# Performance work log

Measured on AMD Instinct MI355X. Metric: run time of the kernel, lower is better.

## Reference

```python
import jax, jax.numpy as jnp
import numpy as np

B, N = 16, 4096

def _fps(xyz, npoint):
    # iterative farthest point sampling on one cloud [n,3] -> [npoint] int32
    n = xyz.shape[0]
    def body(carry, _):
        dist, far = carry
        d = jnp.sum((xyz - xyz[far]) ** 2, axis=-1)
        dist = jnp.minimum(dist, d)
        return (dist, jnp.argmax(dist).astype(jnp.int32)), far
    _, idx = jax.lax.scan(body, (jnp.full((n,), 1e10, jnp.float32), jnp.int32(0)), None, length=npoint)
    return idx

def _ball_query(radius, nsample, xyz, new_xyz):
    # xyz [n,3], new_xyz [S,3] -> [S,nsample] neighbor indices (first-in-index order, as in PointNet++)
    n = xyz.shape[0]
    sqr = jnp.sum((new_xyz[:, None, :] - xyz[None, :, :]) ** 2, axis=-1)  # [S,n]
    idx = jnp.where(sqr > radius * radius, n, jnp.arange(n, dtype=jnp.int32)[None, :])
    idx = jnp.sort(idx, axis=-1)[:, :nsample]
    return jnp.where(idx == n, idx[:, :1], idx)

def _gather(p, i):
    return jax.vmap(lambda pp, ii: pp[ii])(p, i)

def _mlp(x, layers):
    # shared MLP = 1x1 conv over grouped points; BN(eval) folded into (W,b)
    for W, b in layers:
        x = jax.nn.relu(jnp.einsum('bsnc,co->bsno', x, W) + b)
    return x

def _sa(xyz, feats, npoint, radius, nsample, layers):
    fps_idx = jax.vmap(lambda p: _fps(p, npoint))(xyz)            # [B,S]
    new_xyz = _gather(xyz, fps_idx)                                # [B,S,3]
    idx = jax.vmap(lambda p, q: _ball_query(radius, nsample, p, q))(xyz, new_xyz)  # [B,S,ns]
    x = _gather(xyz, idx) - new_xyz[:, :, None, :]                 # centered grouped xyz
    if feats is not None:
        x = jnp.concatenate([x, _gather(feats, idx)], axis=-1)
    x = _mlp(x, layers)
    return new_xyz, jnp.max(x, axis=2)

def _forward(points, w10, b10, w11, b11, w12, b12, w20, b20, w21, b21, w22, b22, w30, b30, w31, b31, w32, b32, lw1, lb1, lw2, lb2, fw1, fb1, fw2, fb2, pos_mean, pos_std, rot_mean, rot_std):
    l1x, l1f = _sa(points, None, 512, 0.2, 32, [(w10, b10), (w11, b11), (w12, b12)])
    l2x, l2f = _sa(l1x, l1f, 128, 0.4, 64, [(w20, b20), (w21, b21), (w22, b22)])
    # sa3: group_all
    x = jnp.concatenate([l2x, l2f], axis=-1)[:, None]              # [B,1,128,259]
    x = _mlp(x, [(w30, b30), (w31, b31), (w32, b32)])
    g = jnp.max(x, axis=2).reshape(points.shape[0], 1024)
    label = jax.nn.sigmoid(jax.nn.relu(g @ lw1 + lb1) @ lw2 + lb2)  # dropout = identity (eval)
    res = jax.nn.relu(g @ fw1 + fb1) @ fw2 + fb2
    pl = res[:, 0:3] * pos_std + pos_mean
    rl = res[:, 3:9] * rot_std + rot_mean
    pr = res[:, 9:12] * pos_std + pos_mean
    rr = res[:, 12:18] * rot_std + rot_mean
    return jnp.concatenate([label, pl, rl, pr, rr], axis=-1)       # [B,20]

def setup_inputs():
    ks = iter(jax.random.split(jax.random.key(0), 64))
    def w(shape, s=0.05):
        return jax.random.normal(next(ks), shape, jnp.float32) * s
    inp = {'points': jax.random.normal(next(ks), (B, N, 3), jnp.float32) * 0.5}
    dims = {'w10': (3, 64), 'w11': (64, 64), 'w12': (64, 128), 'w20': (131, 128), 'w21': (128, 128), 'w22': (128, 256), 'w30': (259, 256), 'w31': (256, 512), 'w32': (512, 1024), 'lw1': (1024, 256), 'lw2': (256, 2), 'fw1': (1024, 512), 'fw2': (512, 18)}
    for name, s in dims.items():
        inp[name] = w(s)
        inp[name.replace('w', 'b', 1)] = jnp.zeros((s[1],), jnp.float32)
    inp['pos_mean'] = w((3,), 0.1)
    inp['pos_std'] = jnp.abs(w((3,))) + 1.0
    inp['rot_mean'] = w((6,), 0.1)
    inp['rot_std'] = jnp.abs(w((6,))) + 1.0
    return inp

def reference(points, w10, b10, w11, b11, w12, b12, w20, b20, w21, b21, w22, b22, w30, b30, w31, b31, w32, b32, lw1, lb1, lw2, lb2, fw1, fb1, fw2, fb2, pos_mean, pos_std, rot_mean, rot_std):
    return _forward(points, w10, b10, w11, b11, w12, b12, w20, b20, w21, b21, w22, b22, w30, b30, w31, b31, w32, b32, lw1, lb1, lw2, lb2, fw1, fb1, fw2, fb2, pos_mean, pos_std, rot_mean, rot_std)
```

## Files before the change

### kernel.cpp

```cpp
#include <hip/hip_runtime.h>
#include <math.h>

#define BB 16
#define NN 4096

typedef float v2f __attribute__((ext_vector_type(2)));
typedef short bfrag8 __attribute__((ext_vector_type(8)));
typedef float fx4 __attribute__((ext_vector_type(4)));

__device__ __forceinline__ v2f pkfma(v2f a, v2f b, v2f c) {
    return __builtin_elementwise_fma(a, b, c);
}

__device__ __forceinline__ fx4 mfma16(bfrag8 a, bfrag8 b, fx4 c) {
    return __builtin_amdgcn_mfma_f32_16x16x32_bf16(a, b, c, 0, 0, 0);
}

__device__ __forceinline__ unsigned short bf16rne(float v) {
    unsigned u = __float_as_uint(v);
    return (unsigned short)((u + 0x7FFFu + ((u >> 16) & 1u)) >> 16);
}
__device__ __forceinline__ void bf16split(float v, unsigned short& h, unsigned short& l) {
    h = bf16rne(v);
    float fh = __uint_as_float((unsigned)h << 16);
    l = bf16rne(v - fh);
}

__device__ __forceinline__ float sq3(float dx, float dy, float dz) {
    return __fadd_rn(__fadd_rn(__fmul_rn(dx, dx), __fmul_rn(dy, dy)), __fmul_rn(dz, dz));
}

template<int CTRL, int RMASK>
__device__ __forceinline__ unsigned long long dpp_max_step(unsigned long long P) {
    int lo = __builtin_amdgcn_update_dpp(0, (int)(unsigned)P,        CTRL, RMASK, 0xf, true);
    int hi = __builtin_amdgcn_update_dpp(0, (int)(unsigned)(P >> 32), CTRL, RMASK, 0xf, true);
    unsigned long long o = ((unsigned long long)(unsigned)hi << 32) | (unsigned)lo;
    return (o > P) ? o : P;
}

__device__ __forceinline__ unsigned long long dpp_wave_max_u64(unsigned long long P) {
    P = dpp_max_step<0x111, 0xf>(P);
    P = dpp_max_step<0x112, 0xf>(P);
    P = dpp_max_step<0x114, 0xf>(P);
    P = dpp_max_step<0x118, 0xf>(P);
    P = dpp_max_step<0x142, 0xa>(P);
    P = dpp_max_step<0x143, 0xc>(P);
    return P;
}

__device__ __forceinline__ unsigned long long u64max(unsigned long long a, unsigned long long b) {
    return (a > b) ? a : b;
}

template<int NPTS, int NPOINT, int TPB>
__global__ __launch_bounds__(TPB) void fps_kernel(const float* __restrict__ xyz,
                                                  float* __restrict__ newxyz,
                                                  float* __restrict__ out_t,
                                                  int ts) {
    constexpr int PPT = NPTS / TPB;
    constexpr int NW  = TPB / 64;
    static_assert(NPOINT <= TPB, "far-history latch needs NPOINT <= TPB");
    __shared__ float sx[NPTS], sy[NPTS], sz[NPTS];
    __shared__ __align__(16) unsigned long long slot[2][NW];
    const int b = blockIdx.x;
    const int tid = threadIdx.x;
    const float* base = xyz + (size_t)b * NPTS * 3;
    for (int i = tid; i < NPTS; i += TPB) {
        sx[i] = base[i * 3 + 0];
        sy[i] = base[i * 3 + 1];
        sz[i] = base[i * 3 + 2];
    }
    __syncthreads();
    float px[PPT], py[PPT], pz[PPT], dist[PPT];
#pragma unroll
    for (int k = 0; k < PPT; k++) {
        int p = tid + k * TPB;
        px[k] = sx[p]; py[k] = sy[p]; pz[k] = sz[p];
        dist[k] = 1e10f;
    }
    int far = 0;
    int myfar = 0;
    const int lane = tid & 63, wid = tid >> 6;
    for (int it = 0; it < NPOINT; it++) {
        if (tid == it) myfar = far;
        float fx = sx[far], fy = sy[far], fz = sz[far];
        float bv = -1.0f; int bi = 0;
#pragma unroll
        for (int k = 0; k < PPT; k++) {
            float d = sq3(px[k] - fx, py[k] - fy, pz[k] - fz);
            float nd = fminf(dist[k], d);
            dist[k] = nd;
            if (nd > bv) { bv = nd; bi = tid + k * TPB; }
        }
        unsigned long long P = ((unsigned long long)__float_as_uint(bv) << 32)
                             | (unsigned long long)(~(unsigned)bi & 0xFFFFFFFFull);
        P = dpp_wave_max_u64(P);
        int bufi = it & 1;
        if (lane == 63) slot[bufi][wid] = P;
        __syncthreads();
        unsigned long long v[NW];
#pragma unroll
        for (int w = 0; w < NW; w++) v[w] = slot[bufi][w];
#pragma unroll
        for (int st = NW / 2; st >= 1; st >>= 1)
#pragma unroll
            for (int w = 0; w < st; w++) v[w] = u64max(v[w], v[w + st]);
        far = (int)(~(unsigned)(v[0] & 0xFFFFFFFFull));
    }
    if (tid < NPOINT) {
        float fx = sx[myfar], fy = sy[myfar], fz = sz[myfar];
        newxyz[((size_t)b * NPOINT + tid) * 3 + 0] = fx;
        newxyz[((size_t)b * NPOINT + tid) * 3 + 1] = fy;
        newxyz[((size_t)b * NPOINT + tid) * 3 + 2] = fz;
        if (out_t) {
            out_t[0 * ts + b * NPOINT + tid] = fx;
            out_t[1 * ts + b * NPOINT + tid] = fy;
            out_t[2 * ts + b * NPOINT + tid] = fz;
        }
    }
}

template<int NS>
__device__ __forceinline__ void bq_body(const float* __restrict__ pts, int n,
                                        const float* __restrict__ centers, int S,
                                        float r2, int* __restrict__ outidx,
                                        int wave, int lane) {
    int b = wave / S, s = wave % S;
    const float* c = centers + ((size_t)b * S + s) * 3;
    float cx = c[0], cy = c[1], cz = c[2];
    const float* pb = pts + (size_t)b * n * 3;
    int* out = outidx + ((size_t)b * S + s) * NS;
    int total = 0, first = -1;
    int rounds = n >> 6;
    for (int r = 0; r < rounds; r++) {
        int p = (r << 6) + lane;
        float dx = pb[p * 3 + 0] - cx, dy = pb[p * 3 + 1] - cy, dz = pb[p * 3 + 2] - cz;
        float d = sq3(dx, dy, dz);
        bool pred = (d <= r2);
        unsigned long long mask = __ballot(pred);
        if (first < 0 && mask) first = (r << 6) + (__ffsll(mask) - 1);
        if (pred) {
            int rank = total + __popcll(mask & ((1ull << lane) - 1ull));
            if (rank < NS) out[rank] = p;
        }
        total += __popcll(mask);
        if (total >= NS) break;
    }
    for (int j = total + lane; j < NS; j += 64) out[j] = first;
}

__global__ __launch_bounds__(512) void bq1_fps2_kernel(const float* __restrict__ points,
                                                       const float* __restrict__ l1x,
                                                       float* __restrict__ l2x,
                                                       float* __restrict__ x3t,
                                                       int* __restrict__ idx1,
                                                       float r2a,
                                                       const float* __restrict__ w21,
                                                       const float* __restrict__ w22,
                                                       float* __restrict__ w21f,
                                                       float* __restrict__ w22f) {
    __shared__ float sx[512], sy[512], sz[512];
    const int tid = threadIdx.x;
    const int lane = tid & 63, wid = tid >> 6;
    if (blockIdx.x < 16) {
        if (wid != 0) return;
        const int b = blockIdx.x;
        const float* base = l1x + (size_t)b * 512 * 3;
        for (int i = lane; i < 512; i += 64) {
            sx[i] = base[i * 3 + 0];
            sy[i] = base[i * 3 + 1];
            sz[i] = base[i * 3 + 2];
        }
        float px[8], py[8], pz[8], dist[8];
#pragma unroll
        for (int k = 0; k < 8; k++) {
            int p = lane + k * 64;
            px[k] = sx[p]; py[k] = sy[p]; pz[k] = sz[p];
            dist[k] = 1e10f;
        }
        int far = 0, myfar0 = 0, myfar1 = 0;
        for (int it = 0; it < 128; it++) {
            if (lane == it) myfar0 = far;
            if (lane == it - 64) myfar1 = far;
            float fx = sx[far], fy = sy[far], fz = sz[far];
            float bv = -1.0f; int bi = 0;
#pragma unroll
            for (int k = 0; k < 8; k++) {
                float d = sq3(px[k] - fx, py[k] - fy, pz[k] - fz);
                float nd = fminf(dist[k], d);
                dist[k] = nd;
                if (nd > bv) { bv = nd; bi = lane + k * 64; }
            }
            unsigned long long P = ((unsigned long long)__float_as_uint(bv) << 32)
                                 | (unsigned long long)(~(unsigned)bi & 0xFFFFFFFFull);
            P = dpp_wave_max_u64(P);
            unsigned lo = (unsigned)__builtin_amdgcn_readlane((int)(unsigned)P, 63);
            far = (int)(~lo);
        }
        {
            int s0 = lane, s1 = lane + 64;
            float a = sx[myfar0], c1 = sy[myfar0], c2 = sz[myfar0];
            l2x[((size_t)b * 128 + s0) * 3 + 0] = a;
            l2x[((size_t)b * 128 + s0) * 3 + 1] = c1;
            l2x[((size_t)b * 128 + s0) * 3 + 2] = c2;
            x3t[0 * 2048 + b * 128 + s0] = a;
            x3t[1 * 2048 + b * 128 + s0] = c1;
            x3t[2 * 2048 + b * 128 + s0] = c2;
            float d = sx[myfar1], e = sy[myfar1], f = sz[myfar1];
            l2x[((size_t)b * 128 + s1) * 3 + 0] = d;
            l2x[((size_t)b * 128 + s1) * 3 + 1] = e;
            l2x[((size_t)b * 128 + s1) * 3 + 2] = f;
            x3t[0 * 2048 + b * 128 + s1] = d;
            x3t[1 * 2048 + b * 128 + s1] = e;
            x3t[2 * 2048 + b * 128 + s1] = f;
        }
    } else if (blockIdx.x < 1040) {
        int wave = (blockIdx.x - 16) * 8 + wid;
        bq_body<32>(points, 4096, l1x, 512, r2a, idx1, wave, lane);
    } else {
        int gt = (blockIdx.x - 1040) * 512 + tid;
        const float* W; float* OF; int NT, N; int t;
        if (gt < 4096) { W = w21; OF = w21f; NT = 8;  N = 128; t = gt; }
        else           { W = w22; OF = w22f; NT = 16; N = 256; t = gt - 4096; }
        int L = t & 63;
        int rest = t >> 6;
        int nt = rest & (NT - 1);
        int hk = (NT == 8) ? (rest >> 3) : (rest >> 4);
        int kt = hk & 3, hl = hk >> 2;
        int k0 = kt * 32 + (L >> 4) * 8;
        int n  = nt * 16 + (L & 15);
        unsigned o[4];
#pragma unroll
        for (int e = 0; e < 4; e++) {
            float va = W[(size_t)(k0 + 2 * e + 0) * N + n];
            float vb = W[(size_t)(k0 + 2 * e + 1) * N + n];
            unsigned short ha, la, hb, lb;
            bf16split(va, ha, la);
            bf16split(vb, hb, lb);
            o[e] = hl ? ((unsigned)la | ((unsigned)lb << 16))
                      : ((unsigned)ha | ((unsigned)hb << 16));
        }
        ((uint4*)OF)[t] = make_uint4(o[0], o[1], o[2], o[3]);
    }
}

__global__ __launch_bounds__(64, 2) void sa1_bq2_kernel(const float* __restrict__ xyz, const float* __restrict__ l1x,
                                                 const int* __restrict__ idx1,
                                                 const float* __restrict__ l2x, int* __restrict__ idx2, float r2b,
                                                 const float* __restrict__ W1, const float* __restrict__ B1,
                                                 const float* __restrict__ W2, const float* __restrict__ B2,
                                                 const float* __restrict__ W3, const float* __restrict__ B3,
                                                 float* __restrict__ l1f) {
    __shared__ float ht[64 * 64];
    int lane = threadIdx.x;
    if (blockIdx.x < 2048) {
        bq_body<64>(l1x, 512, l2x, 128, r2b, idx2, blockIdx.x, lane);
        return;
    }
    int blk = blockIdx.x - 2048;
    int b = blk >> 8;
    int s = ((blk & 255) << 1) | (lane >> 5);
    int nn = lane & 31;
    int center = b * 512 + s;
    int ii = idx1[center * 32 + nn];
    float px = xyz[((size_t)b * NN + ii) * 3 + 0] - l1x[(size_t)center * 3 + 0];
    float py = xyz[((size_t)b * NN + ii) * 3 + 1] - l1x[(size_t)center * 3 + 1];
    float pz = xyz[((size_t)b * NN + ii) * 3 + 2] - l1x[(size_t)center * 3 + 2];
#pragma unroll
    for (int c = 0; c < 64; c++)
        ht[c * 64 + lane] = fmaxf(B1[c] + px * W1[c] + py * W1[64 + c] + pz * W1[128 + c], 0.0f);
    __syncthreads();
    v2f h2[32];
    const v2f* B2v = (const v2f*)B2;
#pragma unroll
    for (int c = 0; c < 32; c++) h2[c] = B2v[c];
    for (int k = 0; k < 64; k++) {
        float xk = ht[k * 64 + lane];
        v2f xk2 = {xk, xk};
        const v2f* wr = (const v2f*)(W2 + k * 64);
#pragma unroll
        for (int c = 0; c < 32; c++) h2[c] = pkfma(xk2, wr[c], h2[c]);
    }
    __syncthreads();
#pragma unroll
    for (int c = 0; c < 32; c++) {
        ht[(2 * c + 0) * 64 + lane] = fmaxf(h2[c].x, 0.0f);
        ht[(2 * c + 1) * 64 + lane] = fmaxf(h2[c].y, 0.0f);
    }
    __syncthreads();
#pragma unroll
    for (int half = 0; half < 2; half++) {
        v2f o[32];
        const v2f* B3v = (const v2f*)(B3 + half * 64);
#pragma unroll
        for (int j = 0; j < 32; j++) o[j] = B3v[j];
        for (int k = 0; k < 64; k++) {
            float xk = ht[k * 64 + lane];
            v2f xk2 = {xk, xk};
            const v2f* wr = (const v2f*)(W3 + k * 128 + half * 64);
#pragma unroll
            for (int j = 0; j < 32; j++) o[j] = pkfma(xk2, wr[j], o[j]);
        }
#pragma unroll
        for (int j = 0; j < 32; j++) {
            float va = fmaxf(o[j].x, 0.0f);
            float vb = fmaxf(o[j].y, 0.0f);
#pragma unroll
            for (int m = 16; m >= 1; m >>= 1) {
                va = fmaxf(va, __shfl_xor(va, m));
                vb = fmaxf(vb, __shfl_xor(vb, m));
            }
            o[j].x = va; o[j].y = vb;
        }
        if (nn == 0) {
#pragma unroll
            for (int j = 0; j < 32; j++) {
                l1f[(size_t)center * 128 + half * 64 + 2 * j + 0] = o[j].x;
                l1f[(size_t)center * 128 + half * 64 + 2 * j + 1] = o[j].y;
            }
        }
    }
}

__global__ __launch_bounds__(256, 4) void sa2_kernel(const float* __restrict__ l1x, const float* __restrict__ l2x,
                                                  const float* __restrict__ l1f, const int* __restrict__ idx2,
                                                  const float* __restrict__ W1, const float* __restrict__ B1,
                                                  const float* __restrict__ w21f, const float* __restrict__ B2,
                                                  const float* __restrict__ w22f, const float* __restrict__ B3,
                                                  float* __restrict__ x3t) {
    __shared__ short hsh[64 * 136];
    __shared__ short hsl[64 * 136];
    int tid = threadIdx.x;
    int w = __builtin_amdgcn_readfirstlane(tid >> 6);
    int lane = tid & 63;
    int b = blockIdx.x >> 7, s = blockIdx.x & 127;
    int center = b * 128 + s;
    int ii = idx2[center * 64 + lane];
    float cx = l2x[(size_t)center * 3 + 0], cy = l2x[(size_t)center * 3 + 1], cz = l2x[(size_t)center * 3 + 2];
    const float* pr = l1x + ((size_t)b * 512 + ii) * 3;
    float px = pr[0] - cx, py = pr[1] - cy, pz = pr[2] - cz;
    const float4* frow = (const float4*)(l1f + ((size_t)b * 512 + ii) * 128);
    v2f h[16];
    {
        const v2f* B1v = (const v2f*)(B1 + w * 32);
        const v2f* w1a = (const v2f*)(W1 + 0 * 128 + w * 32);
        const v2f* w1b = (const v2f*)(W1 + 1 * 128 + w * 32);
        const v2f* w1c = (const v2f*)(W1 + 2 * 128 + w * 32);
        v2f px2 = {px, px}, py2 = {py, py}, pz2 = {pz, pz};
#pragma unroll
        for (int j = 0; j < 16; j++)
            h[j] = pkfma(pz2, w1c[j], pkfma(py2, w1b[j], pkfma(px2, w1a[j], B1v[j])));
    }
#pragma unroll 2
    for (int k4 = 0; k4 < 32; k4++) {
        float4 f = frow[k4];
        const v2f* wr = (const v2f*)(W1 + (3 + k4 * 4) * 128 + w * 32);
        v2f fx2 = {f.x, f.x}, fy2 = {f.y, f.y}, fz2 = {f.z, f.z}, fw2 = {f.w, f.w};
#pragma unroll
        for (int j = 0; j < 16; j++) {
            h[j] = pkfma(fx2, wr[j], h[j]);
            h[j] = pkfma(fy2, wr[64 + j], h[j]);
            h[j] = pkfma(fz2, wr[128 + j], h[j]);
            h[j] = pkfma(fw2, wr[192 + j], h[j]);
        }
    }
#pragma unroll
    for (int j = 0; j < 16; j++) {
        float v0 = fmaxf(h[j].x, 0.0f);
        float v1 = fmaxf(h[j].y, 0.0f);
        unsigned short h0, l0, h1, l1;
        bf16split(v0, h0, l0);
        bf16split(v1, h1, l1);
        int cb = lane * 136 + w * 32 + 2 * j;
        *(unsigned*)(&hsh[cb]) = (unsigned)h0 | ((unsigned)h1 << 16);
        *(unsigned*)(&hsl[cb]) = (unsigned)l0 | ((unsigned)l1 << 16);
    }
    __syncthreads();
    {
        fx4 acc[4][2];
#pragma unroll
        for (int mt = 0; mt < 4; mt++)
#pragma unroll
            for (int nt = 0; nt < 2; nt++) {
                float bn = B2[(2 * w + nt) * 16 + (lane & 15)];
                acc[mt][nt] = (fx4){bn, bn, bn, bn};
            }
#pragma unroll
        for (int kt = 0; kt < 4; kt++) {
            bfrag8 ah[4], al[4];
#pragma unroll
            for (int mt = 0; mt < 4; mt++) {
                int idx = (mt * 16 + (lane & 15)) * 136 + kt * 32 + (lane >> 4) * 8;
                ah[mt] = *(const bfrag8*)(&hsh[idx]);
                al[mt] = *(const bfrag8*)(&hsl[idx]);
            }
#pragma unroll
            for (int nt = 0; nt < 2; nt++) {
                int ng = 2 * w + nt;
                bfrag8 bh = ((const bfrag8*)w21f)[(size_t)((0 + kt) * 8 + ng) * 64 + lane];
                bfrag8 bl = ((const bfrag8*)w21f)[(size_t)((4 + kt) * 8 + ng) * 64 + lane];
#pragma unroll
                for (int mt = 0; mt < 4; mt++) {
                    acc[mt][nt] = mfma16(ah[mt], bh, acc[mt][nt]);
                    acc[mt][nt] = mfma16(ah[mt], bl, acc[mt][nt]);
                    acc[mt][nt] = mfma16(al[mt], bh, acc[mt][nt]);
                }
            }
        }
        __syncthreads();
#pragma unroll
        for (int mt = 0; mt < 4; mt++)
#pragma unroll
            for (int nt = 0; nt < 2; nt++)
#pragma unroll
                for (int r = 0; r < 4; r++) {
                    float v = fmaxf(acc[mt][nt][r], 0.0f);
                    int m = mt * 16 + (lane >> 4) * 4 + r;
                    int n = (2 * w + nt) * 16 + (lane & 15);
                    unsigned short hb, lb;
                    bf16split(v, hb, lb);
                    hsh[m * 136 + n] = (short)hb;
                    hsl[m * 136 + n] = (short)lb;
                }
        __syncthreads();
    }
#pragma unroll 1
    for (int pass = 0; pass < 2; pass++) {
        int nb = w * 4 + pass * 2;
        fx4 acc[4][2];
#pragma unroll
        for (int mt = 0; mt < 4; mt++)
#pragma unroll
            for (int nt = 0; nt < 2; nt++) {
                float bn = B3[(nb + nt) * 16 + (lane & 15)];
                acc[mt][nt] = (fx4){bn, bn, bn, bn};
            }
#pragma unroll
        for (int kt = 0; kt < 4; kt++) {
            bfrag8 ah[4], al[4];
#pragma unroll
            for (int mt = 0; mt < 4; mt++) {
                int idx = (mt * 16 + (lane & 15)) * 136 + kt * 32 + (lane >> 4) * 8;
                ah[mt] = *(const bfrag8*)(&hsh[idx]);
                al[mt] = *(const bfrag8*)(&hsl[idx]);
            }
#pragma unroll
            for (int nt = 0; nt < 2; nt++) {
                bfrag8 bh = ((const bfrag8*)w22f)[(size_t)((0 + kt) * 16 + (nb + nt)) * 64 + lane];
                bfrag8 bl = ((const bfrag8*)w22f)[(size_t)((4 + kt) * 16 + (nb + nt)) * 64 + lane];
#pragma unroll
                for (int mt = 0; mt < 4; mt++) {
                    acc[mt][nt] = mfma16(ah[mt], bh, acc[mt][nt]);
                    acc[mt][nt] = mfma16(ah[mt], bl, acc[mt][nt]);
                    acc[mt][nt] = mfma16(al[mt], bh, acc[mt][nt]);
                }
            }
        }
#pragma unroll
        for (int nt = 0; nt < 2; nt++) {
            float mv = 0.0f;
#pragma unroll
            for (int mt = 0; mt < 4; mt++)
#pragma unroll
                for (int r = 0; r < 4; r++)
                    mv = fmaxf(mv, acc[mt][nt][r]);
            mv = fmaxf(mv, __shfl_xor(mv, 16));
            mv = fmaxf(mv, __shfl_xor(mv, 32));
            if (lane < 16)
                x3t[(size_t)(3 + (nb + nt) * 16 + lane) * 2048 + center] = mv;
        }
    }
}

template<int K, int COUT, int CPT, bool MAXOUT>
__device__ __forceinline__ void gemm_t_body(const float* __restrict__ in_t,
                                            const float* __restrict__ W,
                                            const float* __restrict__ bias,
                                            float* __restrict__ outp,
                                            int bid, int lane) {
    int rw = bid & 31, cg = bid >> 5;
    int row = rw * 64 + lane;
    int cbase = cg * CPT;
    v2f acc[CPT / 2];
    const v2f* bv = (const v2f*)(bias + cbase);
#pragma unroll
    for (int j = 0; j < CPT / 2; j++) acc[j] = bv[j];
    for (int k = 0; k < K; k++) {
        float xk = in_t[(size_t)k * 2048 + row];
        v2f xk2 = {xk, xk};
        const v2f* wr = (const v2f*)(W + (size_t)k * COUT + cbase);
#pragma unroll
        for (int j = 0; j < CPT / 2; j++) acc[j] = pkfma(xk2, wr[j], acc[j]);
    }
    if (MAXOUT) {
        int b = row >> 7;
#pragma unroll
        for (int j = 0; j < CPT / 2; j++) {
            float va = fmaxf(acc[j].x, 0.0f);
            float vb = fmaxf(acc[j].y, 0.0f);
#pragma unroll
            for (int m = 32; m >= 1; m >>= 1) {
                va = fmaxf(va, __shfl_xor(va, m));
                vb = fmaxf(vb, __shfl_xor(vb, m));
            }
            if (lane == 0) {
                atomicMax((int*)(outp + (size_t)b * 1024 + cbase + 2 * j + 0), __float_as_int(va));
                atomicMax((int*)(outp + (size_t)b * 1024 + cbase + 2 * j + 1), __float_as_int(vb));
            }
        }
    } else {
#pragma unroll
        for (int j = 0; j < CPT / 2; j++) {
            outp[(size_t)(cbase + 2 * j + 0) * 2048 + row] = fmaxf(acc[j].x, 0.0f);
            outp[(size_t)(cbase + 2 * j + 1) * 2048 + row] = fmaxf(acc[j].y, 0.0f);
        }
    }
}

template<int K, int COUT, int CPT, bool MAXOUT>
__global__ __launch_bounds__(64, 4) void gemm_t_kernel(const float* __restrict__ in_t,
                                                    const float* __restrict__ W,
                                                    const float* __restrict__ bias,
                                                    float* __restrict__ outp) {
    gemm_t_body<K, COUT, CPT, MAXOUT>(in_t, W, bias, outp, blockIdx.x, threadIdx.x);
}

__global__ __launch_bounds__(64, 4) void gemm1_zerog_kernel(const float* __restrict__ in_t,
                                                            const float* __restrict__ W,
                                                            const float* __restrict__ bias,
                                                            float* __restrict__ outp,
                                                            float* __restrict__ g) {
    if (blockIdx.x < 1024) {
        gemm_t_body<259, 256, 8, false>(in_t, W, bias, outp, blockIdx.x, threadIdx.x);
    } else {
        g[(blockIdx.x - 1024) * 64 + threadIdx.x] = 0.0f;
    }
}

__global__ __launch_bounds__(512) void head_kernel(const float* __restrict__ g,
                                                   const float* __restrict__ lw1, const float* __restrict__ lb1,
                                                   const float* __restrict__ lw2, const float* __restrict__ lb2,
                                                   const float* __restrict__ fw1, const float* __restrict__ fb1,
                                                   const float* __restrict__ fw2, const float* __restrict__ fb2,
                                                   const float* __restrict__ pm, const float* __restrict__ ps,
                                                   const float* __restrict__ rm, const float* __restrict__ rs,
                                                   float* __restrict__ out) {
    __shared__ float gl[1024], a1[256], f1[512];
    int b = blockIdx.x, t = threadIdx.x;
    for (int i = t; i < 1024; i += 512) gl[i] = g[b * 1024 + i];
    __syncthreads();
    {
        float acc = fb1[t];
        for (int k = 0; k < 1024; k++) acc += gl[k] * fw1[k * 512 + t];
        f1[t] = fmaxf(acc, 0.0f);
    }
    if (t < 256) {
        float acc = lb1[t];
        for (int k = 0; k < 1024; k++) acc += gl[k] * lw1[k * 256 + t];
        a1[t] = fmaxf(acc, 0.0f);
    }
    __syncthreads();
    if (t < 2) {
        float z = lb2[t];
        for (int k = 0; k < 256; k++) z += a1[k] * lw2[k * 2 + t];
        out[b * 20 + t] = 1.0f / (1.0f + expf(-z));
    } else if (t < 20) {
        int i = t - 2;
        float z = fb2[i];
        for (int k = 0; k < 512; k++) z += f1[k] * fw2[k * 18 + i];
        float sc, mn;
        if (i < 3)       { sc = ps[i];      mn = pm[i]; }
        else if (i < 9)  { sc = rs[i - 3];  mn = rm[i - 3]; }
        else if (i < 12) { sc = ps[i - 9];  mn = pm[i - 9]; }
        else             { sc = rs[i - 12]; mn = rm[i - 12]; }
        out[b * 20 + t] = z * sc + mn;
    }
}

static inline size_t align256(size_t x) { return (x + 255) & ~(size_t)255; }

extern "C" void kernel_launch(void* const* d_in, const int* in_sizes, int n_in,
                              void* d_out, int out_size, void* d_ws, size_t ws_size,
                              hipStream_t stream) {
    const float* points = (const float*)d_in[0];
    const float* w10 = (const float*)d_in[1];  const float* b10 = (const float*)d_in[2];
    const float* w11 = (const float*)d_in[3];  const float* b11 = (const float*)d_in[4];
    const float* w12 = (const float*)d_in[5];  const float* b12 = (const float*)d_in[6];
    const float* w20 = (const float*)d_in[7];  const float* b20 = (const float*)d_in[8];
    const float* w21 = (const float*)d_in[9];  const float* b21 = (const float*)d_in[10];
    const float* w22 = (const float*)d_in[11]; const float* b22 = (const float*)d_in[12];
    const float* w30 = (const float*)d_in[13]; const float* b30 = (const float*)d_in[14];
    const float* w31 = (const float*)d_in[15]; const float* b31 = (const float*)d_in[16];
    const float* w32 = (const float*)d_in[17]; const float* b32 = (const float*)d_in[18];
    const float* lw1 = (const float*)d_in[19]; const float* lb1 = (const float*)d_in[20];
    const float* lw2 = (const float*)d_in[21]; const float* lb2 = (const float*)d_in[22];
    const float* fw1 = (const float*)d_in[23]; const float* fb1 = (const float*)d_in[24];
    const float* fw2 = (const float*)d_in[25]; const float* fb2 = (const float*)d_in[26];
    const float* pm  = (const float*)d_in[27]; const float* ps  = (const float*)d_in[28];
    const float* rm  = (const float*)d_in[29]; const float* rs  = (const float*)d_in[30];
    float* out = (float*)d_out;

    char* p = (char*)d_ws;
    float* l1x  = (float*)p; p += align256((size_t)BB * 512 * 3 * 4);
    int*   idx1 = (int*)p;   p += align256((size_t)BB * 512 * 32 * 4);
    float* l1f  = (float*)p; p += align256((size_t)BB * 512 * 128 * 4);
    float* l2x  = (float*)p; p += align256((size_t)BB * 128 * 3 * 4);
    int*   idx2 = (int*)p;   p += align256((size_t)BB * 128 * 64 * 4);
    float* x3t  = (float*)p; p += align256((size_t)259 * 2048 * 4);
    float* h1t  = (float*)p; p += align256((size_t)256 * 2048 * 4);
    float* h2t  = (float*)p; p += align256((size_t)512 * 2048 * 4);
    float* g    = (float*)p; p += align256((size_t)BB * 1024 * 4);
    float* w21f = h1t;
    float* w22f = h1t + (size_t)2 * 4 * 8 * 64 * 4;

    const float R2A = (float)(0.2 * 0.2);
    const float R2B = (float)(0.4 * 0.4);

    fps_kernel<4096, 512, 512><<<BB, 512, 0, stream>>>(points, l1x, (float*)nullptr, 0);
    bq1_fps2_kernel<<<1064, 512, 0, stream>>>(points, l1x, l2x, x3t, idx1, R2A, w21, w22, w21f, w22f);
    sa1_bq2_kernel<<<6144, 64, 0, stream>>>(points, l1x, idx1, l2x, idx2, R2B,
                                            w10, b10, w11, b11, w12, b12, l1f);
    sa2_kernel<<<2048, 256, 0, stream>>>(l1x, l2x, l1f, idx2, w20, b20, w21f, b21, w22f, b22, x3t);
    gemm1_zerog_kernel<<<1280, 64, 0, stream>>>(x3t, w30, b30, h1t, g);
    gemm_t_kernel<256, 512, 8, false><<<2048, 64, 0, stream>>>(h1t, w31, b31, h2t);
    gemm_t_kernel<512, 1024, 8, true><<<4096, 64, 0, stream>>>(h2t, w32, b32, g);
    head_kernel<<<BB, 512, 0, stream>>>(g, lw1, lb1, lw2, lb2, fw1, fb1, fw2, fb2, pm, ps, rm, rs, out);
}
```

Measured before the change: 922.4 us.

## Run SA1 shared-MLP layers on bf16x3 MFMA with prepacked split weights

Replaces the per-lane packed-FMA fp32 loops for the second and third SA1 MLP layers with 16x16x32 bf16 MFMA, using a hi/lo bf16 split (three MFMAs per tile) to keep near-fp32 accuracy. Weights w11/w12 are pre-split and packed into fragment layout by extra blocks in the existing bq1 kernel. Activations are staged in padded LDS as hi/lo bf16, and the max-pool over 32 neighbours is done with cross-lane shuffles on the MFMA outputs. This targets the SA1 compute cost but adds split/pack overhead and a small accuracy deviation from fp32.

```diff
diff --git a/kernel.cpp b/kernel.cpp
--- a/kernel.cpp
+++ b/kernel.cpp
@@ -157,8 +157,12 @@
                                                        float r2a,
                                                        const float* __restrict__ w21,
                                                        const float* __restrict__ w22,
+                                                       const float* __restrict__ w11s,
+                                                       const float* __restrict__ w12s,
                                                        float* __restrict__ w21f,
-                                                       float* __restrict__ w22f) {
+                                                       float* __restrict__ w22f,
+                                                       float* __restrict__ w11f,
+                                                       float* __restrict__ w12f) {
     __shared__ float sx[512], sy[512], sz[512];
     const int tid = threadIdx.x;
     const int lane = tid & 63, wid = tid >> 6;
@@ -219,14 +223,16 @@
         bq_body<32>(points, 4096, l1x, 512, r2a, idx1, wave, lane);
     } else {
         int gt = (blockIdx.x - 1040) * 512 + tid;
-        const float* W; float* OF; int NT, N; int t;
-        if (gt < 4096) { W = w21; OF = w21f; NT = 8;  N = 128; t = gt; }
-        else           { W = w22; OF = w22f; NT = 16; N = 256; t = gt - 4096; }
+        const float* W; float* OF; int NT, KT, N; int t;
+        if (gt < 4096)       { W = w21;  OF = w21f; NT = 8;  KT = 4; N = 128; t = gt; }
+        else if (gt < 12288) { W = w22;  OF = w22f; NT = 16; KT = 4; N = 256; t = gt - 4096; }
+        else if (gt < 13312) { W = w11s; OF = w11f; NT = 4;  KT = 2; N = 64;  t = gt - 12288; }
+        else                 { W = w12s; OF = w12f; NT = 8;  KT = 2; N = 128; t = gt - 13312; }
         int L = t & 63;
         int rest = t >> 6;
         int nt = rest & (NT - 1);
-        int hk = (NT == 8) ? (rest >> 3) : (rest >> 4);
-        int kt = hk & 3, hl = hk >> 2;
+        int hk = rest / NT;
+        int kt = hk % KT, hl = hk / KT;
         int k0 = kt * 32 + (L >> 4) * 8;
         int n  = nt * 16 + (L & 15);
         unsigned o[4];
@@ -248,10 +254,11 @@
                                                  const int* __restrict__ idx1,
                                                  const float* __restrict__ l2x, int* __restrict__ idx2, float r2b,
                                                  const float* __restrict__ W1, const float* __restrict__ B1,
-                                                 const float* __restrict__ W2, const float* __restrict__ B2,
-                                                 const float* __restrict__ W3, const float* __restrict__ B3,
+                                                 const float* __restrict__ W2f, const float* __restrict__ B2,
+                                                 const float* __restrict__ W3f, const float* __restrict__ B3,
                                                  float* __restrict__ l1f) {
-    __shared__ float ht[64 * 64];
+    __shared__ short hsh[64 * 72];
+    __shared__ short hsl[64 * 72];
     int lane = threadIdx.x;
     if (blockIdx.x < 2048) {
         bq_body<64>(l1x, 512, l2x, 128, r2b, idx2, blockIdx.x, lane);
@@ -259,65 +266,123 @@
     }
     int blk = blockIdx.x - 2048;
     int b = blk >> 8;
-    int s = ((blk & 255) << 1) | (lane >> 5);
-    int nn = lane & 31;
+    int ct = lane >> 5, nn = lane & 31;
+    int s = ((blk & 255) << 1) | ct;
     int center = b * 512 + s;
+    int c0 = b * 512 + ((blk & 255) << 1);
     int ii = idx1[center * 32 + nn];
     float px = xyz[((size_t)b * NN + ii) * 3 + 0] - l1x[(size_t)center * 3 + 0];
     float py = xyz[((size_t)b * NN + ii) * 3 + 1] - l1x[(size_t)center * 3 + 1];
     float pz = xyz[((size_t)b * NN + ii) * 3 + 2] - l1x[(size_t)center * 3 + 2];
 #pragma unroll
-    for (int c = 0; c < 64; c++)
-        ht[c * 64 + lane] = fmaxf(B1[c] + px * W1[c] + py * W1[64 + c] + pz * W1[128 + c], 0.0f);
+    for (int c2 = 0; c2 < 32; c2++) {
+        int ca = 2 * c2, cb = 2 * c2 + 1;
+        float v0 = fmaxf(B1[ca] + px * W1[ca] + py * W1[64 + ca] + pz * W1[128 + ca], 0.0f);
+        float v1 = fmaxf(B1[cb] + px * W1[cb] + py * W1[64 + cb] + pz * W1[128 + cb], 0.0f);
+        unsigned short h0, l0, h1, l1;
+        bf16split(v0, h0, l0);
+        bf16split(v1, h1, l1);
+        int base = lane * 72 + ca;
+        *(unsigned*)(&hsh[base]) = (unsigned)h0 | ((unsigned)h1 << 16);
+        *(unsigned*)(&hsl[base]) = (unsigned)l0 | ((unsigned)l1 << 16);
+    }
     __syncthreads();
-    v2f h2[32];
-    const v2f* B2v = (const v2f*)B2;
-#pragma unroll
-    for (int c = 0; c < 32; c++) h2[c] = B2v[c];
-    for (int k = 0; k < 64; k++) {
-        float xk = ht[k * 64 + lane];
-        v2f xk2 = {xk, xk};
-        const v2f* wr = (const v2f*)(W2 + k * 64);
-#pragma unroll
-        for (int c = 0; c < 32; c++) h2[c] = pkfma(xk2, wr[c], h2[c]);
-    }
-    __syncthreads();
-#pragma unroll
-    for (int c = 0; c < 32; c++) {
-        ht[(2 * c + 0) * 64 + lane] = fmaxf(h2[c].x, 0.0f);
-        ht[(2 * c + 1) * 64 + lane] = fmaxf(h2[c].y, 0.0f);
-    }
-    __syncthreads();
-#pragma unroll
-    for (int half = 0; half < 2; half++) {
-        v2f o[32];
-        const v2f* B3v = (const v2f*)(B3 + half * 64);
-#pragma unroll
-        for (int j = 0; j < 32; j++) o[j] = B3v[j];
-        for (int k = 0; k < 64; k++) {
-            float xk = ht[k * 64 + lane];
-            v2f xk2 = {xk, xk};
-            const v2f* wr = (const v2f*)(W3 + k * 128 + half * 64);
-#pragma unroll
-            for (int j = 0; j < 32; j++) o[j] = pkfma(xk2, wr[j], o[j]);
-        }
-#pragma unroll
-        for (int j = 0; j < 32; j++) {
-            float va = fmaxf(o[j].x, 0.0f);
-            float vb = fmaxf(o[j].y, 0.0f);
-#pragma unroll
-            for (int m = 16; m >= 1; m >>= 1) {
-                va = fmaxf(va, __shfl_xor(va, m));
-                vb = fmaxf(vb, __shfl_xor(vb, m));
-            }
-            o[j].x = va; o[j].y = vb;
-        }
-        if (nn == 0) {
-#pragma unroll
-            for (int j = 0; j < 32; j++) {
-                l1f[(size_t)center * 128 + half * 64 + 2 * j + 0] = o[j].x;
-                l1f[(size_t)center * 128 + half * 64 + 2 * j + 1] = o[j].y;
-            }
+    {
+        fx4 acc[4][4];
+#pragma unroll
+        for (int mt = 0; mt < 4; mt++)
+#pragma unroll
+            for (int nt = 0; nt < 4; nt++) {
+                float bn = B2[nt * 16 + (lane & 15)];
+                acc[mt][nt] = (fx4){bn, bn, bn, bn};
+            }
+        const bfrag8* w2v = (const bfrag8*)W2f;
+#pragma unroll
+        for (int kt = 0; kt < 2; kt++) {
+            bfrag8 ah[4], al[4];
+#pragma unroll
+            for (int mt = 0; mt < 4; mt++) {
+                int idx = (mt * 16 + (lane & 15)) * 72 + kt * 32 + (lane >> 4) * 8;
+                ah[mt] = *(const bfrag8*)(&hsh[idx]);
+                al[mt] = *(const bfrag8*)(&hsl[idx]);
+            }
+#pragma unroll
+            for (int nt = 0; nt < 4; nt++) {
+                bfrag8 bh = w2v[(size_t)((0 + kt) * 4 + nt) * 64 + lane];
+                bfrag8 bl = w2v[(size_t)((2 + kt) * 4 + nt) * 64 + lane];
+#pragma unroll
+                for (int mt = 0; mt < 4; mt++) {
+                    acc[mt][nt] = mfma16(ah[mt], bh, acc[mt][nt]);
+                    acc[mt][nt] = mfma16(ah[mt], bl, acc[mt][nt]);
+                    acc[mt][nt] = mfma16(al[mt], bh, acc[mt][nt]);
+                }
+            }
+        }
+        __syncthreads();
+#pragma unroll
+        for (int mt = 0; mt < 4; mt++)
+#pragma unroll
+            for (int nt = 0; nt < 4; nt++)
+#pragma unroll
+                for (int r = 0; r < 4; r++) {
+                    float v = fmaxf(acc[mt][nt][r], 0.0f);
+                    int m = mt * 16 + (lane >> 4) * 4 + r;
+                    int n = nt * 16 + (lane & 15);
+                    unsigned short hb, lb;
+                    bf16split(v, hb, lb);
+                    hsh[m * 72 + n] = (short)hb;
+                    hsl[m * 72 + n] = (short)lb;
+                }
+        __syncthreads();
+    }
+    const bfrag8* w3v = (const bfrag8*)W3f;
+#pragma unroll 1
+    for (int pass = 0; pass < 2; pass++) {
+        int nbase = pass * 4;
+        fx4 acc[4][4];
+#pragma unroll
+        for (int mt = 0; mt < 4; mt++)
+#pragma unroll
+            for (int nt = 0; nt < 4; nt++) {
+                float bn = B3[(nbase + nt) * 16 + (lane & 15)];
+                acc[mt][nt] = (fx4){bn, bn, bn, bn};
+            }
+#pragma unroll
+        for (int kt = 0; kt < 2; kt++) {
+            bfrag8 ah[4], al[4];
+#pragma unroll
+            for (int mt = 0; mt < 4; mt++) {
+                int idx = (mt * 16 + (lane & 15)) * 72 + kt * 32 + (lane >> 4) * 8;
+                ah[mt] = *(const bfrag8*)(&hsh[idx]);
+                al[mt] = *(const bfrag8*)(&hsl[idx]);
+            }
+#pragma unroll
+            for (int nt = 0; nt < 4; nt++) {
+                bfrag8 bh = w3v[(size_t)((0 + kt) * 8 + nbase + nt) * 64 + lane];
+                bfrag8 bl = w3v[(size_t)((2 + kt) * 8 + nbase + nt) * 64 + lane];
+#pragma unroll
+                for (int mt = 0; mt < 4; mt++) {
+                    acc[mt][nt] = mfma16(ah[mt], bh, acc[mt][nt]);
+                    acc[mt][nt] = mfma16(ah[mt], bl, acc[mt][nt]);
+                    acc[mt][nt] = mfma16(al[mt], bh, acc[mt][nt]);
+                }
+            }
+        }
+#pragma unroll
+        for (int nt = 0; nt < 4; nt++) {
+            float mv0 = 0.0f, mv1 = 0.0f;
+#pragma unroll
+            for (int r = 0; r < 4; r++) {
+                mv0 = fmaxf(mv0, fmaxf(acc[0][nt][r], acc[1][nt][r]));
+                mv1 = fmaxf(mv1, fmaxf(acc[2][nt][r], acc[3][nt][r]));
+            }
+            mv0 = fmaxf(mv0, __shfl_xor(mv0, 16));
+            mv0 = fmaxf(mv0, __shfl_xor(mv0, 32));
+            mv1 = fmaxf(mv1, __shfl_xor(mv1, 16));
+            mv1 = fmaxf(mv1, __shfl_xor(mv1, 32));
+            int n = (nbase + nt) * 16 + (lane & 15);
+            if (lane < 16)      l1f[(size_t)c0 * 128 + n] = mv0;
+            else if (lane < 32) l1f[(size_t)(c0 + 1) * 128 + n] = mv1;
         }
     }
 }
@@ -611,15 +676,18 @@
     float* h2t  = (float*)p; p += align256((size_t)512 * 2048 * 4);
     float* g    = (float*)p; p += align256((size_t)BB * 1024 * 4);
     float* w21f = h1t;
-    float* w22f = h1t + (size_t)2 * 4 * 8 * 64 * 4;
+    float* w22f = h1t + (size_t)16384;
+    float* w11f = h1t + (size_t)16384 + 32768;
+    float* w12f = h1t + (size_t)16384 + 32768 + 4096;
 
     const float R2A = (float)(0.2 * 0.2);
     const float R2B = (float)(0.4 * 0.4);
 
     fps_kernel<4096, 512, 512><<<BB, 512, 0, stream>>>(points, l1x, (float*)nullptr, 0);
-    bq1_fps2_kernel<<<1064, 512, 0, stream>>>(points, l1x, l2x, x3t, idx1, R2A, w21, w22, w21f, w22f);
+    bq1_fps2_kernel<<<1070, 512, 0, stream>>>(points, l1x, l2x, x3t, idx1, R2A,
+                                              w21, w22, w11, w12, w21f, w22f, w11f, w12f);
     sa1_bq2_kernel<<<6144, 64, 0, stream>>>(points, l1x, idx1, l2x, idx2, R2B,
-                                            w10, b10, w11, b11, w12, b12, l1f);
+                                            w10, b10, w11f, b11, w12f, b12, l1f);
     sa2_kernel<<<2048, 256, 0, stream>>>(l1x, l2x, l1f, idx2, w20, b20, w21f, b21, w22f, b22, x3t);
     gemm1_zerog_kernel<<<1280, 64, 0, stream>>>(x3t, w30, b30, h1t, g);
     gemm_t_kernel<256, 512, 8, false><<<2048, 64, 0, stream>>>(h1t, w31, b31, h2t);
```

Result: faster. 821.8 us (-10.9%).
